# Kernel tuning notes

Measured on AMD Instinct MI355X. Metric: run time of the kernel, lower is better.

The kernel has to match this reference:

```python
import jax, jax.numpy as jnp
import numpy as np

B, N, C_IN, C_OUT, H = 8, 1024, 256, 512, 8
DH = C_OUT // H  # per-head dim
LN_EPS = 1e-5


def setup_inputs() -> dict:
    key = jax.random.key(0)
    ks = jax.random.split(key, 8)
    # xavier_normal std for [in, out] fan pair
    std = float(np.sqrt(2.0 / (C_IN + DH)))
    x = jax.random.normal(ks[0], (B, N, C_IN), dtype=jnp.float32)
    adj = jax.random.uniform(ks[1], (B, N, N), dtype=jnp.float32)
    W_q = jax.random.normal(ks[2], (H, C_IN, DH), dtype=jnp.float32) * std
    W_k = jax.random.normal(ks[3], (H, C_IN, DH), dtype=jnp.float32) * std
    W_v = jax.random.normal(ks[4], (H, C_IN, DH), dtype=jnp.float32) * std
    # Conv1d(in, out, kernel=1) == pointwise linear: weight [out, in], bias [out]
    bound = float(1.0 / np.sqrt(C_IN))
    conv_w = jax.random.uniform(ks[5], (C_OUT, C_IN), dtype=jnp.float32, minval=-bound, maxval=bound)
    conv_b = jax.random.uniform(ks[6], (C_OUT,), dtype=jnp.float32, minval=-bound, maxval=bound)
    ln_w = jnp.ones((C_OUT,), dtype=jnp.float32)
    ln_b = jnp.zeros((C_OUT,), dtype=jnp.float32)
    return {"x": x, "adj": adj, "W_q": W_q, "W_k": W_k, "W_v": W_v,
            "conv_w": conv_w, "conv_b": conv_b, "ln_w": ln_w, "ln_b": ln_b}


def reference(x, adj, W_q, W_k, W_v, conv_w, conv_b, ln_w, ln_b):
    # NOTE: in the original module, adj is used only to compute D_neg/A_hat,
    # which are discarded; it has no effect on the output. Attention is dense.
    dh = W_q.shape[-1]
    scale = 1.0 / jnp.sqrt(jnp.asarray(dh, dtype=x.dtype))
    # batched per-head projections: [B,N,Cin] x [H,Cin,dh] -> [B,H,N,dh]
    Q = jnp.einsum('bni,hio->bhno', x, W_q)
    K = jnp.einsum('bni,hio->bhno', x, W_k)
    V = jnp.einsum('bni,hio->bhno', x, W_v)
    scores = jnp.einsum('bhqd,bhkd->bhqk', Q, K) * scale  # [B,H,N,N]
    attn = jax.nn.softmax(scores, axis=-1)
    out = jax.nn.relu(jnp.einsum('bhqk,bhkd->bhqd', attn, V))  # [B,H,N,dh]
    b, h, n, d = out.shape
    out = out.transpose(0, 2, 1, 3).reshape(b, n, h * d)  # concat heads -> [B,N,Cout]
    # matching_conv: 1x1 conv == linear over channels
    proj = jnp.einsum('bni,oi->bno', x, conv_w) + conv_b
    y = out + proj
    mean = jnp.mean(y, axis=-1, keepdims=True)
    var = jnp.var(y, axis=-1, keepdims=True)
    y = (y - mean) * jax.lax.rsqrt(var + LN_EPS)
    return y * ln_w + ln_b
```

## Files before the change

kernel.cpp:

```cpp
#include <hip/hip_runtime.h>

#define B_ 8
#define N_ 1024
#define CIN_ 256
#define COUT_ 512
#define H_ 8
#define DH_ 64

typedef __attribute__((ext_vector_type(8))) short bf8;
typedef __attribute__((ext_vector_type(4))) short s4;
typedef __attribute__((ext_vector_type(4))) float f4;
typedef __attribute__((ext_vector_type(2))) unsigned int u2;

__device__ __forceinline__ short f2bf(float f) {
  unsigned u = __builtin_bit_cast(unsigned, f);
  u += 0x7fffu + ((u >> 16) & 1u);
  return (short)(u >> 16);
}
__device__ __forceinline__ float bf2f(short s) {
  unsigned u = ((unsigned)(unsigned short)s) << 16;
  return __builtin_bit_cast(float, u);
}

#if __has_builtin(__builtin_amdgcn_exp2f)
#define EXP2 __builtin_amdgcn_exp2f
#else
#define EXP2 exp2f
#endif

__device__ __forceinline__ unsigned cvtpk(float a, float b) {
  unsigned u;
  asm("v_cvt_pk_bf16_f32 %0, %1, %2" : "=v"(u) : "v"(a), "v"(b));
  return u;
}

#define MFMA16(a, b, c) __builtin_amdgcn_mfma_f32_16x16x32_bf16((a), (b), (c), 0, 0, 0)

#define GLD16(gp, lp)                                                              \
  __builtin_amdgcn_global_load_lds((const __attribute__((address_space(1))) void*)(gp), \
                                   (__attribute__((address_space(3))) void*)(lp), 16, 0, 0)

__global__ void k_prep(const float* __restrict__ Wq, const float* __restrict__ Wk,
                       const float* __restrict__ Wv, const float* __restrict__ Cw,
                       const float* __restrict__ x, short* __restrict__ Wt,
                       short* __restrict__ xb) {
  int blk = blockIdx.x;
  if (blk < 2048) {
    int col = blk;
    int k = threadIdx.x;
    float v;
    if (col < 512) {
      int h = col >> 6, d = col & 63;
      v = Wq[(h * CIN_ + k) * DH_ + d];
    } else if (col < 1024) {
      int c = col - 512, h = c >> 6, d = c & 63;
      v = Wk[(h * CIN_ + k) * DH_ + d];
    } else if (col < 1536) {
      int c = col - 1024, h = c >> 6, d = c & 63;
      v = Wv[(h * CIN_ + k) * DH_ + d];
    } else {
      v = Cw[(col - 1536) * CIN_ + k];
    }
    Wt[col * CIN_ + k] = f2bf(v);
  } else {
    int i = (blk - 2048) * 256 + threadIdx.x;
    f4 a = *reinterpret_cast<const f4*>(x + (size_t)i * 8);
    f4 b = *reinterpret_cast<const f4*>(x + (size_t)i * 8 + 4);
    bf8 o;
    o[0] = f2bf(a[0]); o[1] = f2bf(a[1]); o[2] = f2bf(a[2]); o[3] = f2bf(a[3]);
    o[4] = f2bf(b[0]); o[5] = f2bf(b[1]); o[6] = f2bf(b[2]); o[7] = f2bf(b[3]);
    *reinterpret_cast<bf8*>(xb + (size_t)i * 8) = o;
  }
}

__global__ __launch_bounds__(256) void k_gemm(const short* __restrict__ xb, const short* __restrict__ Wt,
                                              short* __restrict__ Qw, short* __restrict__ Kw,
                                              short* __restrict__ Vt, short* __restrict__ Pj) {
  __shared__ short Al[2][128][64];
  __shared__ short Bl[2][128][64];
  int tid = threadIdx.x;
  int mt = blockIdx.x >> 4, nt = blockIdx.x & 15;
  int row0 = mt * 128, col0 = nt * 128;
  int w = tid >> 6, lane = tid & 63, g = lane >> 4, lr = lane & 15;
  int wm = w >> 1, wn = w & 1;
  f4 acc[4][4];
#pragma unroll
  for (int i = 0; i < 4; ++i)
#pragma unroll
    for (int j = 0; j < 4; ++j) acc[i][j] = (f4){0.f, 0.f, 0.f, 0.f};

  int srow[4], sgc[4];
#pragma unroll
  for (int p = 0; p < 4; ++p) {
    int s = p * 256 + tid;
    srow[p] = s >> 3;
    sgc[p] = (s & 7) ^ (srow[p] & 7);
  }

#define STAGE_AB(k0_, buf_)                                                     \
  {                                                                             \
    char* abase = (char*)&Al[buf_][0][0];                                       \
    char* bbase = (char*)&Bl[buf_][0][0];                                       \
    _Pragma("unroll")                                                           \
    for (int p = 0; p < 4; ++p) {                                               \
      int lb = (p * 256 + w * 64) << 4;                                         \
      GLD16(xb + (row0 + srow[p]) * CIN_ + (k0_) + sgc[p] * 8, abase + lb);     \
      GLD16(Wt + (col0 + srow[p]) * CIN_ + (k0_) + sgc[p] * 8, bbase + lb);     \
    }                                                                           \
  }

  STAGE_AB(0, 0);

  for (int kt = 0; kt < 4; ++kt) {
    int cur = kt & 1;
    if (kt < 3) {
      STAGE_AB((kt + 1) * 64, cur ^ 1);
      asm volatile("s_waitcnt vmcnt(8)" ::: "memory");
    } else {
      asm volatile("s_waitcnt vmcnt(0)" ::: "memory");
    }
    __builtin_amdgcn_s_barrier();

    const short* al = &Al[cur][0][0];
    const short* bl = &Bl[cur][0][0];
    bf8 af[4][2], bb[4][2];
#pragma unroll
    for (int mi = 0; mi < 4; ++mi) {
      int R = wm * 64 + mi * 16 + lr;
      int sw = R & 7;
      af[mi][0] = *reinterpret_cast<const bf8*>(al + R * 64 + ((g ^ sw) * 8));
      af[mi][1] = *reinterpret_cast<const bf8*>(al + R * 64 + (((4 + g) ^ sw) * 8));
    }
#pragma unroll
    for (int ni = 0; ni < 4; ++ni) {
      int R = wn * 64 + ni * 16 + lr;
      int sw = R & 7;
      bb[ni][0] = *reinterpret_cast<const bf8*>(bl + R * 64 + ((g ^ sw) * 8));
      bb[ni][1] = *reinterpret_cast<const bf8*>(bl + R * 64 + (((4 + g) ^ sw) * 8));
    }
#pragma unroll
    for (int mi = 0; mi < 4; ++mi)
#pragma unroll
      for (int ni = 0; ni < 4; ++ni) {
        acc[mi][ni] = MFMA16(af[mi][0], bb[ni][0], acc[mi][ni]);
        acc[mi][ni] = MFMA16(af[mi][1], bb[ni][1], acc[mi][ni]);
      }
    asm volatile("s_waitcnt lgkmcnt(0)" ::: "memory");
    __builtin_amdgcn_s_barrier();
  }

  const float QSCL = 0.125f * 1.4426950408889634f;
#pragma unroll
  for (int mi = 0; mi < 4; ++mi)
#pragma unroll
    for (int ni = 0; ni < 4; ++ni) {
      int c = col0 + wn * 64 + ni * 16 + lr;
      int r0 = row0 + wm * 64 + mi * 16 + g * 4;
      int b = r0 >> 10, n0 = r0 & 1023;
      if (c < 1024) {
#pragma unroll
        for (int j = 0; j < 4; ++j) {
          int n = n0 + j;
          if (c < 512) {
            Qw[((b * H_ + (c >> 6)) * N_ + n) * DH_ + (c & 63)] = f2bf(acc[mi][ni][j] * QSCL);
          } else {
            int cc = c - 512;
            Kw[((b * H_ + (cc >> 6)) * N_ + n) * DH_ + (cc & 63)] = f2bf(acc[mi][ni][j]);
          }
        }
      } else if (c < 1536) {
        int cc = c - 1024;
        int hh = cc >> 6, d = cc & 63;
        s4 vv;
#pragma unroll
        for (int j = 0; j < 4; ++j) vv[j] = f2bf(acc[mi][ni][j]);
        *reinterpret_cast<s4*>(Vt + ((size_t)(b * H_ + hh) * DH_ + d) * N_ + n0) = vv;
      } else {
#pragma unroll
        for (int j = 0; j < 4; ++j) {
          Pj[(size_t)(r0 + j) * COUT_ + (c - 1536)] = f2bf(acc[mi][ni][j]);
        }
      }
    }
}

__global__ __launch_bounds__(256) void k_attn(const short* __restrict__ Qw, const short* __restrict__ Kw,
                                              const short* __restrict__ Vt, short* __restrict__ At) {
  __shared__ short Kl[2][64][64];
  __shared__ short Vl[2][64][64];
  __shared__ short Pl[4][2][16][64];
  int tid = threadIdx.x;
  int nid = ((blockIdx.x & 7) << 6) | (blockIdx.x >> 3);
  int bh = nid >> 3;
  int qb = nid & 7;
  int w = tid >> 6, lane = tid & 63, g = lane >> 4, lr = lane & 15;
  int qglob = qb * 128 + w * 32;
  const short* Qp = Qw + ((size_t)bh * N_ + qglob) * DH_;
  const short* Kp = Kw + (size_t)bh * N_ * DH_;
  const short* Vp = Vt + (size_t)bh * DH_ * N_;

  int sr0 = tid >> 3, sc0 = (tid & 7) ^ (sr0 & 7);
  int s1 = tid + 256;
  int sr1 = s1 >> 3, sc1 = (s1 & 7) ^ (sr1 & 7);
  int lo0 = (w * 64) << 4;
  int lo1 = (w * 64 + 256) << 4;

  {
    const short* kb = Kp;
    const short* vb = Vp;
    char* klb = (char*)&Kl[0][0][0];
    char* vlb = (char*)&Vl[0][0][0];
    GLD16(kb + sr0 * 64 + sc0 * 8, klb + lo0);
    GLD16(kb + sr1 * 64 + sc1 * 8, klb + lo1);
    GLD16(vb + (size_t)sr0 * N_ + sc0 * 8, vlb + lo0);
    GLD16(vb + (size_t)sr1 * N_ + sc1 * 8, vlb + lo1);
  }

  bf8 aq[2][2];
#pragma unroll
  for (int qs = 0; qs < 2; ++qs) {
    aq[qs][0] = *reinterpret_cast<const bf8*>(Qp + (qs * 16 + lr) * DH_ + g * 8);
    aq[qs][1] = *reinterpret_cast<const bf8*>(Qp + (qs * 16 + lr) * DH_ + 32 + g * 8);
  }

  f4 o[2][4];
  f4 lacc[2];
#pragma unroll
  for (int qs = 0; qs < 2; ++qs) {
    lacc[qs] = (f4){0.f, 0.f, 0.f, 0.f};
#pragma unroll
    for (int i = 0; i < 4; ++i) o[qs][i] = (f4){0.f, 0.f, 0.f, 0.f};
  }

  const int swz = (lr & 7) << 3;
  short* pl0 = &Pl[w][0][0][0];
  short* pl1 = &Pl[w][1][0][0];

  for (int t = 0; t < 16; ++t) {
    int cur = t & 1;
    if (t < 15) {
      const short* kb = Kp + (t + 1) * (64 * DH_);
      const short* vb = Vp + (t + 1) * 64;
      char* klb = (char*)&Kl[cur ^ 1][0][0];
      char* vlb = (char*)&Vl[cur ^ 1][0][0];
      GLD16(kb + sr0 * 64 + sc0 * 8, klb + lo0);
      GLD16(kb + sr1 * 64 + sc1 * 8, klb + lo1);
      GLD16(vb + (size_t)sr0 * N_ + sc0 * 8, vlb + lo0);
      GLD16(vb + (size_t)sr1 * N_ + sc1 * 8, vlb + lo1);
      asm volatile("s_waitcnt vmcnt(4)" ::: "memory");
    } else {
      asm volatile("s_waitcnt vmcnt(0)" ::: "memory");
    }
    __builtin_amdgcn_s_barrier();

    const short* klc = &Kl[cur][0][0];
    bf8 bk0[4], bk1[4];
#pragma unroll
    for (int kt = 0; kt < 4; ++kt) {
      int R = kt * 16 + lr;
      const short* kr = klc + R * 64;
      int sw = (R & 7) << 3;
      bk0[kt] = *reinterpret_cast<const bf8*>(kr + ((g * 8) ^ sw));
      bk1[kt] = *reinterpret_cast<const bf8*>(kr + ((32 + g * 8) ^ sw));
    }
    f4 s0[4], s1v[4];
#pragma unroll
    for (int kt = 0; kt < 4; ++kt) {
      f4 z = (f4){0.f, 0.f, 0.f, 0.f};
      z = MFMA16(bk0[kt], aq[0][0], z);
      z = MFMA16(bk1[kt], aq[0][1], z);
      s0[kt] = z;
      f4 z2 = (f4){0.f, 0.f, 0.f, 0.f};
      z2 = MFMA16(bk0[kt], aq[1][0], z2);
      z2 = MFMA16(bk1[kt], aq[1][1], z2);
      s1v[kt] = z2;
    }
#pragma unroll
    for (int kt = 0; kt < 4; ++kt) {
      f4 p;
      p[0] = EXP2(s0[kt][0]); p[1] = EXP2(s0[kt][1]);
      p[2] = EXP2(s0[kt][2]); p[3] = EXP2(s0[kt][3]);
      lacc[0] += p;
      u2 pk;
      pk[0] = cvtpk(p[0], p[1]);
      pk[1] = cvtpk(p[2], p[3]);
      *reinterpret_cast<u2*>(pl0 + lr * 64 + ((kt * 16 + g * 4) ^ swz)) = pk;
    }
#pragma unroll
    for (int kt = 0; kt < 4; ++kt) {
      f4 p;
      p[0] = EXP2(s1v[kt][0]); p[1] = EXP2(s1v[kt][1]);
      p[2] = EXP2(s1v[kt][2]); p[3] = EXP2(s1v[kt][3]);
      lacc[1] += p;
      u2 pk;
      pk[0] = cvtpk(p[0], p[1]);
      pk[1] = cvtpk(p[2], p[3]);
      *reinterpret_cast<u2*>(pl1 + lr * 64 + ((kt * 16 + g * 4) ^ swz)) = pk;
    }
    asm volatile("s_waitcnt lgkmcnt(0)" ::: "memory");
    __builtin_amdgcn_sched_barrier(0);
    bf8 pa00 = *reinterpret_cast<const bf8*>(pl0 + lr * 64 + ((g * 8) ^ swz));
    bf8 pa01 = *reinterpret_cast<const bf8*>(pl0 + lr * 64 + ((32 + g * 8) ^ swz));
    bf8 pa10 = *reinterpret_cast<const bf8*>(pl1 + lr * 64 + ((g * 8) ^ swz));
    bf8 pa11 = *reinterpret_cast<const bf8*>(pl1 + lr * 64 + ((32 + g * 8) ^ swz));
    const short* vlc = &Vl[cur][0][0];
#pragma unroll
    for (int dt = 0; dt < 4; ++dt) {
      int R = dt * 16 + lr;
      const short* vr = vlc + R * 64;
      int sw = (R & 7) << 3;
      bf8 bv0 = *reinterpret_cast<const bf8*>(vr + ((g * 8) ^ sw));
      bf8 bv1 = *reinterpret_cast<const bf8*>(vr + ((32 + g * 8) ^ sw));
      o[0][dt] = MFMA16(pa00, bv0, o[0][dt]);
      o[0][dt] = MFMA16(pa01, bv1, o[0][dt]);
      o[1][dt] = MFMA16(pa10, bv0, o[1][dt]);
      o[1][dt] = MFMA16(pa11, bv1, o[1][dt]);
    }
    asm volatile("s_waitcnt lgkmcnt(0)" ::: "memory");
    __builtin_amdgcn_s_barrier();
  }

  float ls[2];
#pragma unroll
  for (int qs = 0; qs < 2; ++qs) {
    float v = (lacc[qs][0] + lacc[qs][1]) + (lacc[qs][2] + lacc[qs][3]);
    v += __shfl_xor(v, 16, 64);
    v += __shfl_xor(v, 32, 64);
    ls[qs] = v;
  }
  float lf[2][4];
#pragma unroll
  for (int qs = 0; qs < 2; ++qs)
#pragma unroll
    for (int j = 0; j < 4; ++j)
      lf[qs][j] = __shfl(ls[qs], (lane & 48) + ((lane & 48) >> 2) + j, 64);
  int b = bh >> 3, h = bh & 7;
#pragma unroll
  for (int qs = 0; qs < 2; ++qs)
#pragma unroll
    for (int dt = 0; dt < 4; ++dt)
#pragma unroll
      for (int j = 0; j < 4; ++j) {
        float v = fmaxf(o[qs][dt][j] / lf[qs][j], 0.f);
        int n = qglob + qs * 16 + g * 4 + j;
        At[((size_t)b * N_ + n) * COUT_ + h * DH_ + dt * 16 + lr] = f2bf(v);
      }
}

__global__ __launch_bounds__(256) void k_ln(const short* __restrict__ At, const short* __restrict__ Pj,
                                            const float* __restrict__ cb, const float* __restrict__ lw,
                                            const float* __restrict__ lb, float* __restrict__ out) {
  int row = blockIdx.x * 4 + (threadIdx.x >> 6);
  int lane = threadIdx.x & 63;
  int c0 = lane * 8;
  bf8 a8 = *reinterpret_cast<const bf8*>(At + (size_t)row * COUT_ + c0);
  bf8 p8 = *reinterpret_cast<const bf8*>(Pj + (size_t)row * COUT_ + c0);
  float y[8];
  float sum = 0.f, sq = 0.f;
#pragma unroll
  for (int j = 0; j < 8; ++j) {
    float v = bf2f(a8[j]) + bf2f(p8[j]) + cb[c0 + j];
    y[j] = v;
    sum += v;
    sq += v * v;
  }
#pragma unroll
  for (int off = 1; off < 64; off <<= 1) {
    sum += __shfl_xor(sum, off, 64);
    sq += __shfl_xor(sq, off, 64);
  }
  float mean = sum * (1.f / 512.f);
  float var = sq * (1.f / 512.f) - mean * mean;
  float rstd = rsqrtf(var + 1e-5f);
  f4 o0, o1;
#pragma unroll
  for (int j = 0; j < 4; ++j) o0[j] = (y[j] - mean) * rstd * lw[c0 + j] + lb[c0 + j];
#pragma unroll
  for (int j = 0; j < 4; ++j) o1[j] = (y[4 + j] - mean) * rstd * lw[c0 + 4 + j] + lb[c0 + 4 + j];
  *reinterpret_cast<f4*>(out + (size_t)row * COUT_ + c0) = o0;
  *reinterpret_cast<f4*>(out + (size_t)row * COUT_ + c0 + 4) = o1;
}

extern "C" void kernel_launch(void* const* d_in, const int* in_sizes, int n_in,
                              void* d_out, int out_size, void* d_ws, size_t ws_size,
                              hipStream_t stream) {
  const float* x  = (const float*)d_in[0];
  const float* Wq = (const float*)d_in[2];
  const float* Wk = (const float*)d_in[3];
  const float* Wv = (const float*)d_in[4];
  const float* Cw = (const float*)d_in[5];
  const float* cb = (const float*)d_in[6];
  const float* lw = (const float*)d_in[7];
  const float* lb = (const float*)d_in[8];
  float* out = (float*)d_out;
  char* ws = (char*)d_ws;
  short* xb = (short*)(ws);
  short* Wt = (short*)(ws + (size_t)4194304);
  short* Qw = (short*)(ws + (size_t)5242880);
  short* Kw = (short*)(ws + (size_t)13631488);
  short* Vt = (short*)(ws + (size_t)22020096);
  short* Pj = (short*)(ws + (size_t)30408704);
  short* At = (short*)(ws + (size_t)38797312);

  hipLaunchKernelGGL(k_prep, dim3(3072), dim3(256), 0, stream, Wq, Wk, Wv, Cw, x, Wt, xb);
  hipLaunchKernelGGL(k_gemm, dim3(1024), dim3(256), 0, stream, xb, Wt, Qw, Kw, Vt, Pj);
  hipLaunchKernelGGL(k_attn, dim3(512), dim3(256), 0, stream, Qw, Kw, Vt, At);
  hipLaunchKernelGGL(k_ln, dim3(2048), dim3(256), 0, stream, At, Pj, cb, lw, lb, out);
}
```

Before: 66.08 us.

## Double per-wave query rows in attention to halve K/V tile reloads

```diff
diff --git a/kernel.cpp b/kernel.cpp
--- a/kernel.cpp
+++ b/kernel.cpp
@@ -184,17 +184,17 @@
     }
 }
 
-__global__ __launch_bounds__(256) void k_attn(const short* __restrict__ Qw, const short* __restrict__ Kw,
-                                              const short* __restrict__ Vt, short* __restrict__ At) {
+__global__ __launch_bounds__(256, 1) void k_attn(const short* __restrict__ Qw, const short* __restrict__ Kw,
+                                                 const short* __restrict__ Vt, short* __restrict__ At) {
   __shared__ short Kl[2][64][64];
   __shared__ short Vl[2][64][64];
-  __shared__ short Pl[4][2][16][64];
+  __shared__ short Pl[4][4][16][64];
   int tid = threadIdx.x;
-  int nid = ((blockIdx.x & 7) << 6) | (blockIdx.x >> 3);
-  int bh = nid >> 3;
-  int qb = nid & 7;
+  int nid = ((blockIdx.x & 7) << 5) | (blockIdx.x >> 3);
+  int bh = nid >> 2;
+  int qb = nid & 3;
   int w = tid >> 6, lane = tid & 63, g = lane >> 4, lr = lane & 15;
-  int qglob = qb * 128 + w * 32;
+  int qglob = qb * 256 + w * 64;
   const short* Qp = Qw + ((size_t)bh * N_ + qglob) * DH_;
   const short* Kp = Kw + (size_t)bh * N_ * DH_;
   const short* Vp = Vt + (size_t)bh * DH_ * N_;
@@ -206,35 +206,58 @@
   int lo1 = (w * 64 + 256) << 4;
 
   {
-    const short* kb = Kp;
-    const short* vb = Vp;
     char* klb = (char*)&Kl[0][0][0];
     char* vlb = (char*)&Vl[0][0][0];
-    GLD16(kb + sr0 * 64 + sc0 * 8, klb + lo0);
-    GLD16(kb + sr1 * 64 + sc1 * 8, klb + lo1);
-    GLD16(vb + (size_t)sr0 * N_ + sc0 * 8, vlb + lo0);
-    GLD16(vb + (size_t)sr1 * N_ + sc1 * 8, vlb + lo1);
-  }
-
-  bf8 aq[2][2];
-#pragma unroll
-  for (int qs = 0; qs < 2; ++qs) {
+    GLD16(Kp + sr0 * 64 + sc0 * 8, klb + lo0);
+    GLD16(Kp + sr1 * 64 + sc1 * 8, klb + lo1);
+    GLD16(Vp + (size_t)sr0 * N_ + sc0 * 8, vlb + lo0);
+    GLD16(Vp + (size_t)sr1 * N_ + sc1 * 8, vlb + lo1);
+  }
+
+  bf8 aq[4][2];
+#pragma unroll
+  for (int qs = 0; qs < 4; ++qs) {
     aq[qs][0] = *reinterpret_cast<const bf8*>(Qp + (qs * 16 + lr) * DH_ + g * 8);
     aq[qs][1] = *reinterpret_cast<const bf8*>(Qp + (qs * 16 + lr) * DH_ + 32 + g * 8);
   }
 
-  f4 o[2][4];
-  f4 lacc[2];
-#pragma unroll
-  for (int qs = 0; qs < 2; ++qs) {
+  f4 o[4][4];
+  f4 lacc[4];
+#pragma unroll
+  for (int qs = 0; qs < 4; ++qs) {
     lacc[qs] = (f4){0.f, 0.f, 0.f, 0.f};
 #pragma unroll
     for (int i = 0; i < 4; ++i) o[qs][i] = (f4){0.f, 0.f, 0.f, 0.f};
   }
 
   const int swz = (lr & 7) << 3;
-  short* pl0 = &Pl[w][0][0][0];
-  short* pl1 = &Pl[w][1][0][0];
+  short* plq0 = &Pl[w][0][0][0];
+  short* plq1 = &Pl[w][1][0][0];
+  short* plq2 = &Pl[w][2][0][0];
+  short* plq3 = &Pl[w][3][0][0];
+
+#define QS_BLOCK(qs_, pl_)                                                      \
+  {                                                                             \
+    f4 s_[4];                                                                   \
+    _Pragma("unroll")                                                           \
+    for (int kt = 0; kt < 4; ++kt) {                                            \
+      f4 z = (f4){0.f, 0.f, 0.f, 0.f};                                          \
+      z = MFMA16(bk0[kt], aq[qs_][0], z);                                       \
+      z = MFMA16(bk1[kt], aq[qs_][1], z);                                       \
+      s_[kt] = z;                                                               \
+    }                                                                           \
+    _Pragma("unroll")                                                           \
+    for (int kt = 0; kt < 4; ++kt) {                                            \
+      f4 p;                                                                     \
+      p[0] = EXP2(s_[kt][0]); p[1] = EXP2(s_[kt][1]);                           \
+      p[2] = EXP2(s_[kt][2]); p[3] = EXP2(s_[kt][3]);                           \
+      lacc[qs_] += p;                                                           \
+      u2 pk;                                                                    \
+      pk[0] = cvtpk(p[0], p[1]);                                                \
+      pk[1] = cvtpk(p[2], p[3]);                                                \
+      *reinterpret_cast<u2*>((pl_) + lr * 64 + ((kt * 16 + g * 4) ^ swz)) = pk; \
+    }                                                                           \
+  }
 
   for (int t = 0; t < 16; ++t) {
     int cur = t & 1;
@@ -263,46 +286,23 @@
       bk0[kt] = *reinterpret_cast<const bf8*>(kr + ((g * 8) ^ sw));
       bk1[kt] = *reinterpret_cast<const bf8*>(kr + ((32 + g * 8) ^ sw));
     }
-    f4 s0[4], s1v[4];
-#pragma unroll
-    for (int kt = 0; kt < 4; ++kt) {
-      f4 z = (f4){0.f, 0.f, 0.f, 0.f};
-      z = MFMA16(bk0[kt], aq[0][0], z);
-      z = MFMA16(bk1[kt], aq[0][1], z);
-      s0[kt] = z;
-      f4 z2 = (f4){0.f, 0.f, 0.f, 0.f};
-      z2 = MFMA16(bk0[kt], aq[1][0], z2);
-      z2 = MFMA16(bk1[kt], aq[1][1], z2);
-      s1v[kt] = z2;
-    }
-#pragma unroll
-    for (int kt = 0; kt < 4; ++kt) {
-      f4 p;
-      p[0] = EXP2(s0[kt][0]); p[1] = EXP2(s0[kt][1]);
-      p[2] = EXP2(s0[kt][2]); p[3] = EXP2(s0[kt][3]);
-      lacc[0] += p;
-      u2 pk;
-      pk[0] = cvtpk(p[0], p[1]);
-      pk[1] = cvtpk(p[2], p[3]);
-      *reinterpret_cast<u2*>(pl0 + lr * 64 + ((kt * 16 + g * 4) ^ swz)) = pk;
-    }
-#pragma unroll
-    for (int kt = 0; kt < 4; ++kt) {
-      f4 p;
-      p[0] = EXP2(s1v[kt][0]); p[1] = EXP2(s1v[kt][1]);
-      p[2] = EXP2(s1v[kt][2]); p[3] = EXP2(s1v[kt][3]);
-      lacc[1] += p;
-      u2 pk;
-      pk[0] = cvtpk(p[0], p[1]);
-      pk[1] = cvtpk(p[2], p[3]);
-      *reinterpret_cast<u2*>(pl1 + lr * 64 + ((kt * 16 + g * 4) ^ swz)) = pk;
-    }
+
+    QS_BLOCK(0, plq0)
+    QS_BLOCK(1, plq1)
+    QS_BLOCK(2, plq2)
+    QS_BLOCK(3, plq3)
+
     asm volatile("s_waitcnt lgkmcnt(0)" ::: "memory");
     __builtin_amdgcn_sched_barrier(0);
-    bf8 pa00 = *reinterpret_cast<const bf8*>(pl0 + lr * 64 + ((g * 8) ^ swz));
-    bf8 pa01 = *reinterpret_cast<const bf8*>(pl0 + lr * 64 + ((32 + g * 8) ^ swz));
-    bf8 pa10 = *reinterpret_cast<const bf8*>(pl1 + lr * 64 + ((g * 8) ^ swz));
-    bf8 pa11 = *reinterpret_cast<const bf8*>(pl1 + lr * 64 + ((32 + g * 8) ^ swz));
+    bf8 pa00 = *reinterpret_cast<const bf8*>(plq0 + lr * 64 + ((g * 8) ^ swz));
+    bf8 pa01 = *reinterpret_cast<const bf8*>(plq0 + lr * 64 + ((32 + g * 8) ^ swz));
+    bf8 pa10 = *reinterpret_cast<const bf8*>(plq1 + lr * 64 + ((g * 8) ^ swz));
+    bf8 pa11 = *reinterpret_cast<const bf8*>(plq1 + lr * 64 + ((32 + g * 8) ^ swz));
+    bf8 pa20 = *reinterpret_cast<const bf8*>(plq2 + lr * 64 + ((g * 8) ^ swz));
+    bf8 pa21 = *reinterpret_cast<const bf8*>(plq2 + lr * 64 + ((32 + g * 8) ^ swz));
+    bf8 pa30 = *reinterpret_cast<const bf8*>(plq3 + lr * 64 + ((g * 8) ^ swz));
+    bf8 pa31 = *reinterpret_cast<const bf8*>(plq3 + lr * 64 + ((32 + g * 8) ^ swz));
+
     const short* vlc = &Vl[cur][0][0];
 #pragma unroll
     for (int dt = 0; dt < 4; ++dt) {
@@ -315,28 +315,32 @@
       o[0][dt] = MFMA16(pa01, bv1, o[0][dt]);
       o[1][dt] = MFMA16(pa10, bv0, o[1][dt]);
       o[1][dt] = MFMA16(pa11, bv1, o[1][dt]);
+      o[2][dt] = MFMA16(pa20, bv0, o[2][dt]);
+      o[2][dt] = MFMA16(pa21, bv1, o[2][dt]);
+      o[3][dt] = MFMA16(pa30, bv0, o[3][dt]);
+      o[3][dt] = MFMA16(pa31, bv1, o[3][dt]);
     }
     asm volatile("s_waitcnt lgkmcnt(0)" ::: "memory");
     __builtin_amdgcn_s_barrier();
   }
 
-  float ls[2];
-#pragma unroll
-  for (int qs = 0; qs < 2; ++qs) {
+  float ls[4];
+#pragma unroll
+  for (int qs = 0; qs < 4; ++qs) {
     float v = (lacc[qs][0] + lacc[qs][1]) + (lacc[qs][2] + lacc[qs][3]);
     v += __shfl_xor(v, 16, 64);
     v += __shfl_xor(v, 32, 64);
     ls[qs] = v;
   }
-  float lf[2][4];
-#pragma unroll
-  for (int qs = 0; qs < 2; ++qs)
+  float lf[4][4];
+#pragma unroll
+  for (int qs = 0; qs < 4; ++qs)
 #pragma unroll
     for (int j = 0; j < 4; ++j)
       lf[qs][j] = __shfl(ls[qs], (lane & 48) + ((lane & 48) >> 2) + j, 64);
   int b = bh >> 3, h = bh & 7;
 #pragma unroll
-  for (int qs = 0; qs < 2; ++qs)
+  for (int qs = 0; qs < 4; ++qs)
 #pragma unroll
     for (int dt = 0; dt < 4; ++dt)
 #pragma unroll
@@ -404,6 +408,6 @@
 
   hipLaunchKernelGGL(k_prep, dim3(3072), dim3(256), 0, stream, Wq, Wk, Wv, Cw, x, Wt, xb);
   hipLaunchKernelGGL(k_gemm, dim3(1024), dim3(256), 0, stream, xb, Wt, Qw, Kw, Vt, Pj);
-  hipLaunchKernelGGL(k_attn, dim3(512), dim3(256), 0, stream, Qw, Kw, Vt, At);
+  hipLaunchKernelGGL(k_attn, dim3(256), dim3(256), 0, stream, Qw, Kw, Vt, At);
   hipLaunchKernelGGL(k_ln, dim3(2048), dim3(256), 0, stream, At, Pj, cb, lw, lb, out);
 }
```

After: 70.54 us. +6.7%, slower.

## Deepen K/V prefetch to four LDS buffers, drop trailing barrier, raise MFMA priority

Applied to the files above, without the earlier changes.

```diff
diff --git a/kernel.cpp b/kernel.cpp
--- a/kernel.cpp
+++ b/kernel.cpp
@@ -186,8 +186,8 @@
 
 __global__ __launch_bounds__(256) void k_attn(const short* __restrict__ Qw, const short* __restrict__ Kw,
                                               const short* __restrict__ Vt, short* __restrict__ At) {
-  __shared__ short Kl[2][64][64];
-  __shared__ short Vl[2][64][64];
+  __shared__ short Kl[4][64][64];
+  __shared__ short Vl[4][64][64];
   __shared__ short Pl[4][2][16][64];
   int tid = threadIdx.x;
   int nid = ((blockIdx.x & 7) << 6) | (blockIdx.x >> 3);
@@ -205,16 +205,20 @@
   int lo0 = (w * 64) << 4;
   int lo1 = (w * 64 + 256) << 4;
 
-  {
-    const short* kb = Kp;
-    const short* vb = Vp;
-    char* klb = (char*)&Kl[0][0][0];
-    char* vlb = (char*)&Vl[0][0][0];
-    GLD16(kb + sr0 * 64 + sc0 * 8, klb + lo0);
-    GLD16(kb + sr1 * 64 + sc1 * 8, klb + lo1);
-    GLD16(vb + (size_t)sr0 * N_ + sc0 * 8, vlb + lo0);
-    GLD16(vb + (size_t)sr1 * N_ + sc1 * 8, vlb + lo1);
-  }
+#define STAGE_KV(tt_, buf_)                                                     \
+  {                                                                             \
+    const short* kb = Kp + (tt_) * (64 * DH_);                                  \
+    const short* vb = Vp + (tt_) * 64;                                          \
+    char* klb = (char*)&Kl[buf_][0][0];                                         \
+    char* vlb = (char*)&Vl[buf_][0][0];                                         \
+    GLD16(kb + sr0 * 64 + sc0 * 8, klb + lo0);                                  \
+    GLD16(kb + sr1 * 64 + sc1 * 8, klb + lo1);                                  \
+    GLD16(vb + (size_t)sr0 * N_ + sc0 * 8, vlb + lo0);                          \
+    GLD16(vb + (size_t)sr1 * N_ + sc1 * 8, vlb + lo1);                          \
+  }
+
+  STAGE_KV(0, 0);
+  STAGE_KV(1, 1);
 
   bf8 aq[2][2];
 #pragma unroll
@@ -237,16 +241,11 @@
   short* pl1 = &Pl[w][1][0][0];
 
   for (int t = 0; t < 16; ++t) {
-    int cur = t & 1;
-    if (t < 15) {
-      const short* kb = Kp + (t + 1) * (64 * DH_);
-      const short* vb = Vp + (t + 1) * 64;
-      char* klb = (char*)&Kl[cur ^ 1][0][0];
-      char* vlb = (char*)&Vl[cur ^ 1][0][0];
-      GLD16(kb + sr0 * 64 + sc0 * 8, klb + lo0);
-      GLD16(kb + sr1 * 64 + sc1 * 8, klb + lo1);
-      GLD16(vb + (size_t)sr0 * N_ + sc0 * 8, vlb + lo0);
-      GLD16(vb + (size_t)sr1 * N_ + sc1 * 8, vlb + lo1);
+    int cur = t & 3;
+    if (t < 14) {
+      STAGE_KV(t + 2, (t + 2) & 3);
+      asm volatile("s_waitcnt vmcnt(8)" ::: "memory");
+    } else if (t == 14) {
       asm volatile("s_waitcnt vmcnt(4)" ::: "memory");
     } else {
       asm volatile("s_waitcnt vmcnt(0)" ::: "memory");
@@ -264,6 +263,7 @@
       bk1[kt] = *reinterpret_cast<const bf8*>(kr + ((32 + g * 8) ^ sw));
     }
     f4 s0[4], s1v[4];
+    __builtin_amdgcn_s_setprio(1);
 #pragma unroll
     for (int kt = 0; kt < 4; ++kt) {
       f4 z = (f4){0.f, 0.f, 0.f, 0.f};
@@ -275,6 +275,7 @@
       z2 = MFMA16(bk1[kt], aq[1][1], z2);
       s1v[kt] = z2;
     }
+    __builtin_amdgcn_s_setprio(0);
 #pragma unroll
     for (int kt = 0; kt < 4; ++kt) {
       f4 p;
@@ -311,13 +312,14 @@
       int sw = (R & 7) << 3;
       bf8 bv0 = *reinterpret_cast<const bf8*>(vr + ((g * 8) ^ sw));
       bf8 bv1 = *reinterpret_cast<const bf8*>(vr + ((32 + g * 8) ^ sw));
+      __builtin_amdgcn_s_setprio(1);
       o[0][dt] = MFMA16(pa00, bv0, o[0][dt]);
       o[0][dt] = MFMA16(pa01, bv1, o[0][dt]);
       o[1][dt] = MFMA16(pa10, bv0, o[1][dt]);
       o[1][dt] = MFMA16(pa11, bv1, o[1][dt]);
+      __builtin_amdgcn_s_setprio(0);
     }
     asm volatile("s_waitcnt lgkmcnt(0)" ::: "memory");
-    __builtin_amdgcn_s_barrier();
   }
 
   float ls[2];
```

Result: no change. 65.64 us (-0.7%).

## Halve attention query tile per block to double grid and add MFMA priority

Applied to the files above, without the earlier changes.

```diff
diff --git a/kernel.cpp b/kernel.cpp
--- a/kernel.cpp
+++ b/kernel.cpp
@@ -184,17 +184,17 @@
     }
 }
 
-__global__ __launch_bounds__(256) void k_attn(const short* __restrict__ Qw, const short* __restrict__ Kw,
-                                              const short* __restrict__ Vt, short* __restrict__ At) {
+__global__ __launch_bounds__(256, 4) void k_attn(const short* __restrict__ Qw, const short* __restrict__ Kw,
+                                                 const short* __restrict__ Vt, short* __restrict__ At) {
   __shared__ short Kl[2][64][64];
   __shared__ short Vl[2][64][64];
-  __shared__ short Pl[4][2][16][64];
+  __shared__ short Pl[4][16][64];
   int tid = threadIdx.x;
-  int nid = ((blockIdx.x & 7) << 6) | (blockIdx.x >> 3);
-  int bh = nid >> 3;
-  int qb = nid & 7;
+  int nid = ((blockIdx.x & 7) << 7) | (blockIdx.x >> 3);
+  int bh = nid >> 4;
+  int qb = nid & 15;
   int w = tid >> 6, lane = tid & 63, g = lane >> 4, lr = lane & 15;
-  int qglob = qb * 128 + w * 32;
+  int qglob = qb * 64 + w * 16;
   const short* Qp = Qw + ((size_t)bh * N_ + qglob) * DH_;
   const short* Kp = Kw + (size_t)bh * N_ * DH_;
   const short* Vp = Vt + (size_t)bh * DH_ * N_;
@@ -206,35 +206,24 @@
   int lo1 = (w * 64 + 256) << 4;
 
   {
-    const short* kb = Kp;
-    const short* vb = Vp;
     char* klb = (char*)&Kl[0][0][0];
     char* vlb = (char*)&Vl[0][0][0];
-    GLD16(kb + sr0 * 64 + sc0 * 8, klb + lo0);
-    GLD16(kb + sr1 * 64 + sc1 * 8, klb + lo1);
-    GLD16(vb + (size_t)sr0 * N_ + sc0 * 8, vlb + lo0);
-    GLD16(vb + (size_t)sr1 * N_ + sc1 * 8, vlb + lo1);
-  }
-
-  bf8 aq[2][2];
-#pragma unroll
-  for (int qs = 0; qs < 2; ++qs) {
-    aq[qs][0] = *reinterpret_cast<const bf8*>(Qp + (qs * 16 + lr) * DH_ + g * 8);
-    aq[qs][1] = *reinterpret_cast<const bf8*>(Qp + (qs * 16 + lr) * DH_ + 32 + g * 8);
-  }
-
-  f4 o[2][4];
-  f4 lacc[2];
-#pragma unroll
-  for (int qs = 0; qs < 2; ++qs) {
-    lacc[qs] = (f4){0.f, 0.f, 0.f, 0.f};
-#pragma unroll
-    for (int i = 0; i < 4; ++i) o[qs][i] = (f4){0.f, 0.f, 0.f, 0.f};
-  }
+    GLD16(Kp + sr0 * 64 + sc0 * 8, klb + lo0);
+    GLD16(Kp + sr1 * 64 + sc1 * 8, klb + lo1);
+    GLD16(Vp + (size_t)sr0 * N_ + sc0 * 8, vlb + lo0);
+    GLD16(Vp + (size_t)sr1 * N_ + sc1 * 8, vlb + lo1);
+  }
+
+  bf8 aq0 = *reinterpret_cast<const bf8*>(Qp + lr * DH_ + g * 8);
+  bf8 aq1 = *reinterpret_cast<const bf8*>(Qp + lr * DH_ + 32 + g * 8);
+
+  f4 o[4];
+  f4 lacc = (f4){0.f, 0.f, 0.f, 0.f};
+#pragma unroll
+  for (int i = 0; i < 4; ++i) o[i] = (f4){0.f, 0.f, 0.f, 0.f};
 
   const int swz = (lr & 7) << 3;
-  short* pl0 = &Pl[w][0][0][0];
-  short* pl1 = &Pl[w][1][0][0];
+  short* pl = &Pl[w][0][0];
 
   for (int t = 0; t < 16; ++t) {
     int cur = t & 1;
@@ -263,46 +252,31 @@
       bk0[kt] = *reinterpret_cast<const bf8*>(kr + ((g * 8) ^ sw));
       bk1[kt] = *reinterpret_cast<const bf8*>(kr + ((32 + g * 8) ^ sw));
     }
-    f4 s0[4], s1v[4];
+    f4 s[4];
+    __builtin_amdgcn_s_setprio(1);
 #pragma unroll
     for (int kt = 0; kt < 4; ++kt) {
       f4 z = (f4){0.f, 0.f, 0.f, 0.f};
-      z = MFMA16(bk0[kt], aq[0][0], z);
-      z = MFMA16(bk1[kt], aq[0][1], z);
-      s0[kt] = z;
-      f4 z2 = (f4){0.f, 0.f, 0.f, 0.f};
-      z2 = MFMA16(bk0[kt], aq[1][0], z2);
-      z2 = MFMA16(bk1[kt], aq[1][1], z2);
-      s1v[kt] = z2;
-    }
+      z = MFMA16(bk0[kt], aq0, z);
+      z = MFMA16(bk1[kt], aq1, z);
+      s[kt] = z;
+    }
+    __builtin_amdgcn_s_setprio(0);
 #pragma unroll
     for (int kt = 0; kt < 4; ++kt) {
       f4 p;
-      p[0] = EXP2(s0[kt][0]); p[1] = EXP2(s0[kt][1]);
-      p[2] = EXP2(s0[kt][2]); p[3] = EXP2(s0[kt][3]);
-      lacc[0] += p;
+      p[0] = EXP2(s[kt][0]); p[1] = EXP2(s[kt][1]);
+      p[2] = EXP2(s[kt][2]); p[3] = EXP2(s[kt][3]);
+      lacc += p;
       u2 pk;
       pk[0] = cvtpk(p[0], p[1]);
       pk[1] = cvtpk(p[2], p[3]);
-      *reinterpret_cast<u2*>(pl0 + lr * 64 + ((kt * 16 + g * 4) ^ swz)) = pk;
-    }
-#pragma unroll
-    for (int kt = 0; kt < 4; ++kt) {
-      f4 p;
-      p[0] = EXP2(s1v[kt][0]); p[1] = EXP2(s1v[kt][1]);
-      p[2] = EXP2(s1v[kt][2]); p[3] = EXP2(s1v[kt][3]);
-      lacc[1] += p;
-      u2 pk;
-      pk[0] = cvtpk(p[0], p[1]);
-      pk[1] = cvtpk(p[2], p[3]);
-      *reinterpret_cast<u2*>(pl1 + lr * 64 + ((kt * 16 + g * 4) ^ swz)) = pk;
+      *reinterpret_cast<u2*>(pl + lr * 64 + ((kt * 16 + g * 4) ^ swz)) = pk;
     }
     asm volatile("s_waitcnt lgkmcnt(0)" ::: "memory");
     __builtin_amdgcn_sched_barrier(0);
-    bf8 pa00 = *reinterpret_cast<const bf8*>(pl0 + lr * 64 + ((g * 8) ^ swz));
-    bf8 pa01 = *reinterpret_cast<const bf8*>(pl0 + lr * 64 + ((32 + g * 8) ^ swz));
-    bf8 pa10 = *reinterpret_cast<const bf8*>(pl1 + lr * 64 + ((g * 8) ^ swz));
-    bf8 pa11 = *reinterpret_cast<const bf8*>(pl1 + lr * 64 + ((32 + g * 8) ^ swz));
+    bf8 pa0 = *reinterpret_cast<const bf8*>(pl + lr * 64 + ((g * 8) ^ swz));
+    bf8 pa1 = *reinterpret_cast<const bf8*>(pl + lr * 64 + ((32 + g * 8) ^ swz));
     const short* vlc = &Vl[cur][0][0];
 #pragma unroll
     for (int dt = 0; dt < 4; ++dt) {
@@ -311,40 +285,31 @@
       int sw = (R & 7) << 3;
       bf8 bv0 = *reinterpret_cast<const bf8*>(vr + ((g * 8) ^ sw));
       bf8 bv1 = *reinterpret_cast<const bf8*>(vr + ((32 + g * 8) ^ sw));
-      o[0][dt] = MFMA16(pa00, bv0, o[0][dt]);
-      o[0][dt] = MFMA16(pa01, bv1, o[0][dt]);
-      o[1][dt] = MFMA16(pa10, bv0, o[1][dt]);
-      o[1][dt] = MFMA16(pa11, bv1, o[1][dt]);
+      __builtin_amdgcn_s_setprio(1);
+      o[dt] = MFMA16(pa0, bv0, o[dt]);
+      o[dt] = MFMA16(pa1, bv1, o[dt]);
+      __builtin_amdgcn_s_setprio(0);
     }
     asm volatile("s_waitcnt lgkmcnt(0)" ::: "memory");
     __builtin_amdgcn_s_barrier();
   }
 
-  float ls[2];
-#pragma unroll
-  for (int qs = 0; qs < 2; ++qs) {
-    float v = (lacc[qs][0] + lacc[qs][1]) + (lacc[qs][2] + lacc[qs][3]);
-    v += __shfl_xor(v, 16, 64);
-    v += __shfl_xor(v, 32, 64);
-    ls[qs] = v;
-  }
-  float lf[2][4];
-#pragma unroll
-  for (int qs = 0; qs < 2; ++qs)
-#pragma unroll
-    for (int j = 0; j < 4; ++j)
-      lf[qs][j] = __shfl(ls[qs], (lane & 48) + ((lane & 48) >> 2) + j, 64);
+  float ls = (lacc[0] + lacc[1]) + (lacc[2] + lacc[3]);
+  ls += __shfl_xor(ls, 16, 64);
+  ls += __shfl_xor(ls, 32, 64);
+  float lf[4];
+#pragma unroll
+  for (int j = 0; j < 4; ++j)
+    lf[j] = __shfl(ls, (lane & 48) + ((lane & 48) >> 2) + j, 64);
   int b = bh >> 3, h = bh & 7;
 #pragma unroll
-  for (int qs = 0; qs < 2; ++qs)
-#pragma unroll
-    for (int dt = 0; dt < 4; ++dt)
-#pragma unroll
-      for (int j = 0; j < 4; ++j) {
-        float v = fmaxf(o[qs][dt][j] / lf[qs][j], 0.f);
-        int n = qglob + qs * 16 + g * 4 + j;
-        At[((size_t)b * N_ + n) * COUT_ + h * DH_ + dt * 16 + lr] = f2bf(v);
-      }
+  for (int dt = 0; dt < 4; ++dt)
+#pragma unroll
+    for (int j = 0; j < 4; ++j) {
+      float v = fmaxf(o[dt][j] / lf[j], 0.f);
+      int n = qglob + g * 4 + j;
+      At[((size_t)b * N_ + n) * COUT_ + h * DH_ + dt * 16 + lr] = f2bf(v);
+    }
 }
 
 __global__ __launch_bounds__(256) void k_ln(const short* __restrict__ At, const short* __restrict__ Pj,
@@ -404,6 +369,6 @@
 
   hipLaunchKernelGGL(k_prep, dim3(3072), dim3(256), 0, stream, Wq, Wk, Wv, Cw, x, Wt, xb);
   hipLaunchKernelGGL(k_gemm, dim3(1024), dim3(256), 0, stream, xb, Wt, Qw, Kw, Vt, Pj);
-  hipLaunchKernelGGL(k_attn, dim3(512), dim3(256), 0, stream, Qw, Kw, Vt, At);
+  hipLaunchKernelGGL(k_attn, dim3(1024), dim3(256), 0, stream, Qw, Kw, Vt, At);
   hipLaunchKernelGGL(k_ln, dim3(2048), dim3(256), 0, stream, At, Pj, cb, lw, lb, out);
 }
```

Result: slower. 67.48 us (+2.1%).
